# Performance work log

Measured on AMD Instinct MI355X. Metric: run time of the kernel, lower is better.

Reference implementation:

```python
import jax, jax.numpy as jnp
import numpy as np

D = 1024   # visual_dim
N = 64     # num_phrases(1) * topN(64)
DEG = 16   # edges per subject row (incl. one guaranteed via a permutation)
E = N * DEG
T = 2      # cfg.MODEL.RELATION.VISUAL_GRAPH_PASSING_TIME


def _graph():
    rng = np.random.default_rng(0)
    perm = rng.permutation(N)
    mask = np.zeros((N, N), bool)
    for i in range(N):
        mask[i, perm[i]] = True  # permutation guarantees every column is covered
        pool = np.delete(np.arange(N), perm[i])
        mask[i, rng.choice(pool, DEG - 1, replace=False)] = True
    hdim, wdim = np.nonzero(mask)  # row-major, exactly E entries
    conn = np.full((N, N), -1, np.int32)
    conn[hdim, wdim] = np.arange(hdim.shape[0])
    edge_idx = hdim * N + wdim  # original: hdim*topN + wdim (topN == N since num_phrases == 1)
    return conn, edge_idx.astype(np.int32)


def setup_inputs():
    conn, edge_idx = _graph()
    key = jax.random.key(0)
    ks = jax.random.split(key, 16)
    p = lambda k, shp: jax.random.normal(k, shp, jnp.float32) * 0.02
    return {
        'visual_feat': jax.random.normal(ks[0], (N, D), jnp.float32),
        'rel_visual_feat': jax.random.normal(ks[1], (E, D), jnp.float32),
        'conn_map': jnp.asarray(conn),
        'topN_boxes_ids': jnp.arange(N, dtype=jnp.int32)[None, :],  # only shape is used
        'edge_idx': jnp.asarray(edge_idx),
        'W_sub': p(ks[2], (D, D)),
        'W_obj': p(ks[3], (D, D)),
        'W_r2s': p(ks[4], (D, D)),
        'W_r2o': p(ks[5], (D, D)),
        'W_joint': p(ks[6], (D, 4 * D)),
        'W_ctx': p(ks[7], (D, 3 * D)),
        'W_rel_update': p(ks[8], (D, 3 * D)),
        'W_rel_joint': p(ks[9], (D, 4 * D)),
        'W_rel_ctx': p(ks[10], (D, 2 * D)),
        'W_node': p(ks[11], (D, 2 * D)),
        'b_node': jnp.zeros((D,), jnp.float32),
        'W_factor': p(ks[12], (D, 2 * D)),
    }


def _forward(visual_feat, rel_visual_feat, conn_map, edge_idx,
             W_sub, W_obj, W_r2s, W_r2o, W_joint, W_ctx, W_rel_update,
             W_rel_joint, W_rel_ctx, W_node, b_node, W_factor):
    n, d = visual_feat.shape
    scale = jnp.asarray(d, visual_feat.dtype) ** 0.5
    connected = conn_map >= 0
    # scatter edge features into the dense [N, N, D] grid
    rel_temp = (jnp.zeros((n * n, d), visual_feat.dtype)
                .at[edge_idx].set(rel_visual_feat)
                .reshape(n, n, d))
    rel_ctx = rel_temp
    vctx = visual_feat
    for _ in range(T):
        # joint node embedding  [N, D]
        vj = jnp.concatenate([visual_feat, vctx, visual_feat * vctx, vctx - visual_feat], 1) @ W_joint.T
        # joint edge embedding  [N, N, D] (1x1 conv == per-position linear)
        rj = jnp.einsum('ijd,od->ijo',
                        jnp.concatenate([rel_temp, rel_ctx, rel_temp * rel_ctx, rel_temp - rel_ctx], 2),
                        W_rel_joint)
        # node -> edge: cat(sub_tile, obj_tile, rj) @ W_rel_update, done without tiling
        Ws, Wo, Wr = W_rel_update[:, :d], W_rel_update[:, d:2 * d], W_rel_update[:, 2 * d:]
        rel_j = (vj @ Ws.T)[:, None, :] + (vj @ Wo.T)[None, :, :] + jnp.einsum('ijd,od->ijo', rj, Wr)
        # edge -> node attention scores (elementwise product of 1x1-conv outputs, summed over channels)
        s_sbj = jnp.einsum('id,ijd->ij', vj @ W_sub.T, jnp.einsum('ijd,od->ijo', rel_j, W_r2s)) / scale
        s_obj = jnp.einsum('jd,ijd->ij', vj @ W_obj.T, jnp.einsum('ijd,od->ijo', rel_j, W_r2o)) / scale
        w_sbj = jax.nn.softmax(jnp.where(connected, s_sbj, -jnp.inf), axis=1)
        w_obj = jax.nn.softmax(jnp.where(connected, s_obj, -jnp.inf), axis=0)
        ctx = jnp.concatenate([jnp.einsum('ijd,ij->id', rel_j, w_sbj),
                               jnp.einsum('ijd,ij->jd', rel_j, w_obj)], 1)
        vctx = jnp.concatenate([vctx, ctx], 1) @ W_ctx.T
        rel_ctx = jnp.einsum('ijd,od->ijo', jnp.concatenate([rel_ctx, rel_j], 2), W_rel_ctx)
    # gather back the valid edges and produce outputs
    rel_out = jnp.concatenate([rel_visual_feat, rel_ctx.reshape(-1, d)[edge_idx]], 1) @ W_factor.T
    v_out = jnp.concatenate([visual_feat, vctx], 1) @ W_node.T + b_node
    deg = connected.sum(1) + connected.sum(0)
    v_out = jnp.where((deg == 0)[:, None], visual_feat, v_out)  # isolated nodes pass through
    return rel_out, v_out


def reference(visual_feat, rel_visual_feat, conn_map, topN_boxes_ids, edge_idx,
              W_sub, W_obj, W_r2s, W_r2o, W_joint, W_ctx, W_rel_update,
              W_rel_joint, W_rel_ctx, W_node, b_node, W_factor):
    del topN_boxes_ids  # only its shape is used in the original
    return _forward(visual_feat, rel_visual_feat, conn_map, edge_idx,
                    W_sub, W_obj, W_r2s, W_r2o, W_joint, W_ctx, W_rel_update,
                    W_rel_joint, W_rel_ctx, W_node, b_node, W_factor)
```

## Files before the change

### kernel.cpp

```cpp
#include <hip/hip_runtime.h>

static constexpr int kN = 64;
static constexpr int kD = 1024;
static constexpr int kE = 1024;
static constexpr int kT = 2;

typedef short  bf16x8 __attribute__((ext_vector_type(8)));
typedef float  f32x4  __attribute__((ext_vector_type(4)));
typedef unsigned short us8 __attribute__((ext_vector_type(8)));
typedef unsigned short us4 __attribute__((ext_vector_type(4)));

__device__ __forceinline__ unsigned short f2b(float f) {
    unsigned int u = __builtin_bit_cast(unsigned int, f);
    u += 0x7FFFu + ((u >> 16) & 1u);
    return (unsigned short)(u >> 16);
}
__device__ __forceinline__ float b2f(unsigned short u) {
    unsigned int x = ((unsigned int)u) << 16;
    return __builtin_bit_cast(float, x);
}
__device__ __forceinline__ bf16x8 cvt8(float4 a, float4 b) {
    us8 o;
    o[0] = f2b(a.x); o[1] = f2b(a.y); o[2] = f2b(a.z); o[3] = f2b(a.w);
    o[4] = f2b(b.x); o[5] = f2b(b.y); o[6] = f2b(b.z); o[7] = f2b(b.w);
    return __builtin_bit_cast(bf16x8, o);
}

struct ASrc { const unsigned short* s0; const unsigned short* s1; const unsigned short* s2; int mode; };

__device__ __forceinline__ bf16x8 loadA8(const ASrc& s, int row, int kg) {
    const int seg = kg >> 10, k = kg & 1023;
    const size_t ro = (size_t)row * 1024 + k;
    if (s.mode == 1) {
        const unsigned short* p = (seg == 0) ? s.s0 : (seg == 1 ? s.s1 : s.s2);
        return *(const bf16x8*)(p + ro);
    }
    const bf16x8 a = *(const bf16x8*)(s.s0 + ro);
    if (seg == 0) return a;
    const bf16x8 b = *(const bf16x8*)(s.s1 + ro);
    const us8 ua = __builtin_bit_cast(us8, a), ub = __builtin_bit_cast(us8, b);
    us8 o;
#pragma unroll
    for (int q = 0; q < 8; ++q) o[q] = f2b(b2f(ua[q]) * b2f(ub[q]));
    return __builtin_bit_cast(bf16x8, o);
}

struct GJob { ASrc a; const unsigned short* W; int ldw; void* P; int M; int K; int KS; int pbf; };
struct GJobs { GJob j[5]; int t0[6]; int nj; };

__global__ __launch_bounds__(256)
void k_gemm(GJobs G)
{
    __shared__ unsigned short lds[16896];
    const int flat = blockIdx.x;
    int ji = 0;
    while (ji + 1 < G.nj && flat >= G.t0[ji + 1]) ++ji;
    const GJob J = G.j[ji];
    const int local = flat - G.t0[ji];
    const int tid = threadIdx.x, lane = tid & 63, wid = tid >> 6;
    const int l15 = lane & 15, l4 = lane >> 4;
    const int sr = tid >> 3, sc8 = tid & 7;
    const int wc8 = (sc8 ^ (sr & 7)) * 8;

    if (J.M >= 128) {
        const int rowTiles = J.M >> 7;
        const int rt = local % rowTiles;
        const int rest = local / rowTiles;
        const int ct = rest & 7, z = rest >> 3;
        const int rowBase = rt * 128, colBase = ct * 128;
        const int kchunk = J.K / J.KS, kbeg = z * kchunk, kend = kbeg + kchunk;
        const int wr = wid >> 1, wc = wid & 1;

        f32x4 acc[4][4] = {};
        bf16x8 ra[4], rb[4];
        auto stage = [&](int kt) {
#pragma unroll
            for (int h = 0; h < 4; ++h) {
                ra[h] = loadA8(J.a, rowBase + sr + 32 * h, kt + sc8 * 8);
                rb[h] = *(const bf16x8*)(J.W + (size_t)(colBase + sr + 32 * h) * J.ldw + kt + sc8 * 8);
            }
        };

        stage(kbeg);
        for (int kt = kbeg; kt < kend; kt += 64) {
            __syncthreads();
#pragma unroll
            for (int h = 0; h < 4; ++h) {
                *(bf16x8*)&lds[(sr + 32 * h) * 64 + wc8] = ra[h];
                *(bf16x8*)&lds[8192 + (sr + 32 * h) * 64 + wc8] = rb[h];
            }
            __syncthreads();
            if (kt + 64 < kend) stage(kt + 64);
#pragma unroll
            for (int kk = 0; kk < 2; ++kk) {
                bf16x8 af[4], bv[4];
#pragma unroll
                for (int m = 0; m < 4; ++m) {
                    const int ar = wr * 64 + m * 16 + l15;
                    af[m] = *(const bf16x8*)&lds[ar * 64 + (((kk << 2) | l4) ^ (ar & 7)) * 8];
                }
#pragma unroll
                for (int n = 0; n < 4; ++n) {
                    const int br = wc * 64 + n * 16 + l15;
                    bv[n] = *(const bf16x8*)&lds[8192 + br * 64 + (((kk << 2) | l4) ^ (br & 7)) * 8];
                }
#pragma unroll
                for (int m = 0; m < 4; ++m)
#pragma unroll
                    for (int n = 0; n < 4; ++n)
                        acc[m][n] = __builtin_amdgcn_mfma_f32_16x16x32_bf16(af[m], bv[n], acc[m][n], 0, 0, 0);
            }
        }

        __syncthreads();
#pragma unroll
        for (int m = 0; m < 4; ++m)
#pragma unroll
            for (int n = 0; n < 4; ++n)
#pragma unroll
                for (int r = 0; r < 4; ++r)
                    lds[(wr * 64 + m * 16 + l4 * 4 + r) * 132 + wc * 64 + n * 16 + l15] =
                        f2b(acc[m][n][r]);
        __syncthreads();
        unsigned short* Pb = (unsigned short*)J.P + (size_t)z * J.M * 1024;
#pragma unroll
        for (int c = tid; c < 2048; c += 256) {
            const int row = c >> 4, ch = c & 15;
            *(bf16x8*)(Pb + (size_t)(rowBase + row) * 1024 + colBase + ch * 8) =
                *(const bf16x8*)&lds[row * 132 + ch * 8];
        }
    } else {
        const int ct = local & 7, z = local >> 3;
        const int colBase = ct * 128;
        const int kchunk = J.K / J.KS, kbeg = z * kchunk, kend = kbeg + kchunk;
        const int wr = wid >> 1, wc = wid & 1;

        bf16x8 ra[2], rb[4];
        auto stage = [&](int kt) {
#pragma unroll
            for (int h = 0; h < 2; ++h)
                ra[h] = loadA8(J.a, sr + 32 * h, kt + sc8 * 8);
#pragma unroll
            for (int h = 0; h < 4; ++h)
                rb[h] = *(const bf16x8*)(J.W + (size_t)(colBase + sr + 32 * h) * J.ldw + kt + sc8 * 8);
        };

        f32x4 acc[2][4] = {};
        stage(kbeg);
        for (int kt = kbeg; kt < kend; kt += 64) {
            __syncthreads();
#pragma unroll
            for (int h = 0; h < 2; ++h)
                *(bf16x8*)&lds[(sr + 32 * h) * 64 + wc8] = ra[h];
#pragma unroll
            for (int h = 0; h < 4; ++h)
                *(bf16x8*)&lds[4096 + (sr + 32 * h) * 64 + wc8] = rb[h];
            __syncthreads();
            if (kt + 64 < kend) stage(kt + 64);
#pragma unroll
            for (int kk = 0; kk < 2; ++kk) {
                const int c8 = kk * 4 + l4;
                bf16x8 af[2], bv[4];
#pragma unroll
                for (int m = 0; m < 2; ++m) {
                    const int ar = wr * 32 + m * 16 + l15;
                    af[m] = *(const bf16x8*)&lds[ar * 64 + (c8 ^ (ar & 7)) * 8];
                }
#pragma unroll
                for (int n = 0; n < 4; ++n) {
                    const int br = wc * 64 + n * 16 + l15;
                    bv[n] = *(const bf16x8*)&lds[4096 + br * 64 + (c8 ^ (br & 7)) * 8];
                }
#pragma unroll
                for (int m = 0; m < 2; ++m)
#pragma unroll
                    for (int n = 0; n < 4; ++n)
                        acc[m][n] = __builtin_amdgcn_mfma_f32_16x16x32_bf16(af[m], bv[n], acc[m][n], 0, 0, 0);
            }
        }
        float* base = (float*)J.P + (size_t)z * J.M * 1024;
#pragma unroll
        for (int m = 0; m < 2; ++m) {
            const int row = wr * 32 + m * 16 + l4 * 4;
#pragma unroll
            for (int n = 0; n < 4; ++n) {
                const int col = colBase + wc * 64 + n * 16 + l15;
#pragma unroll
                for (int r = 0; r < 4; ++r)
                    base[(size_t)(row + r) * 1024 + col] = acc[m][n][r];
            }
        }
    }
}

struct RJob { const void* P; int MO8; int KS; int pbf; float* Cf; unsigned short* Cb;
              const unsigned short* addb; const float* bias; int gather; };
struct RJobs { RJob j[6]; int t0[7]; int nj; const int* eidx; const float* gP; int gKS; };

__global__ void k_reduce(RJobs R)
{
    const int flat = blockIdx.x;
    int ji = 0;
    while (ji + 1 < R.nj && flat >= R.t0[ji + 1]) ++ji;
    const RJob J = R.j[ji];
    const int i8 = (flat - R.t0[ji]) * 256 + threadIdx.x;
    if (i8 >= J.MO8) return;
    float s[8] = {0.f, 0.f, 0.f, 0.f, 0.f, 0.f, 0.f, 0.f};
    if (J.pbf) {
        const unsigned short* P = (const unsigned short*)J.P;
        for (int z = 0; z < J.KS; ++z) {
            const us8 v = *(const us8*)(P + (size_t)z * J.MO8 * 8 + (size_t)i8 * 8);
#pragma unroll
            for (int q = 0; q < 8; ++q) s[q] += b2f(v[q]);
        }
    } else {
        const float* P = (const float*)J.P;
        for (int z = 0; z < J.KS; ++z) {
            const float* p = P + (size_t)z * J.MO8 * 8 + (size_t)i8 * 8;
            const float4 v0 = *(const float4*)p;
            const float4 v1 = *(const float4*)(p + 4);
            s[0] += v0.x; s[1] += v0.y; s[2] += v0.z; s[3] += v0.w;
            s[4] += v1.x; s[5] += v1.y; s[6] += v1.z; s[7] += v1.w;
        }
    }
    if (J.addb) {
        const us8 v = *(const us8*)(J.addb + (size_t)i8 * 8);
#pragma unroll
        for (int q = 0; q < 8; ++q) s[q] += b2f(v[q]);
    }
    if (J.gather) {
        const int e = i8 >> 7, c8 = i8 & 127;
        const int idx = R.eidx[e];
        const float* as_ = R.gP + (size_t)(idx >> 6) * 1024 + c8 * 8;
        const float* ao_ = R.gP + 131072 + (size_t)(idx & 63) * 1024 + c8 * 8;
        for (int z = 0; z < R.gKS; ++z) {
#pragma unroll
            for (int q = 0; q < 8; ++q)
                s[q] += as_[(size_t)z * 65536 + q] + ao_[(size_t)z * 65536 + q];
        }
    }
    if (J.bias) {
        const int c8 = i8 & 127;
#pragma unroll
        for (int q = 0; q < 8; ++q) s[q] += J.bias[c8 * 8 + q];
    }
    if (J.Cf) {
        *(float4*)(J.Cf + (size_t)i8 * 8)     = make_float4(s[0], s[1], s[2], s[3]);
        *(float4*)(J.Cf + (size_t)i8 * 8 + 4) = make_float4(s[4], s[5], s[6], s[7]);
    }
    if (J.Cb) {
        us8 o;
#pragma unroll
        for (int q = 0; q < 8; ++q) o[q] = f2b(s[q]);
        *(us8*)(J.Cb + (size_t)i8 * 8) = o;
    }
}

struct ConvBatch { const float* s[7]; unsigned short* d[7]; int beg8[7]; int total8; };
__global__ void k_f2b_batch(ConvBatch cb)
{
    int i = blockIdx.x * blockDim.x + threadIdx.x;
    if (i >= cb.total8) return;
    int k = 0;
    while (k < 6 && i >= cb.beg8[k + 1]) ++k;
    const int j = i - cb.beg8[k];
    const float4 v0 = reinterpret_cast<const float4*>(cb.s[k])[2 * j];
    const float4 v1 = reinterpret_cast<const float4*>(cb.s[k])[2 * j + 1];
    const bf16x8 o = cvt8(v0, v1);
    *(bf16x8*)(cb.d[k] + (size_t)j * 8) = o;
}

struct T4 { const float* s[4]; unsigned short* d[4]; };
__global__ __launch_bounds__(256)
void k_transpose(T4 t4)
{
    __shared__ float tile[64][65];
    const float* __restrict__ src = t4.s[blockIdx.z];
    unsigned short* __restrict__ dst = t4.d[blockIdx.z];
    const int bx = blockIdx.x * 64, by = blockIdx.y * 64;
    const int c = threadIdx.x & 63, r0 = threadIdx.x >> 6;
#pragma unroll
    for (int h = 0; h < 16; ++h) {
        const int r = r0 * 16 + h;
        tile[r][c] = src[(size_t)(by + r) * 1024 + bx + c];
    }
    __syncthreads();
#pragma unroll
    for (int h = 0; h < 16; ++h) {
        const int kk = r0 * 16 + h;
        dst[(size_t)(bx + kk) * 1024 + by + c] = f2b(tile[c][kk]);
    }
}

__global__ __launch_bounds__(256)
void k_buildW(const float* __restrict__ Wrel, const float* __restrict__ Wjnt,
              unsigned short* __restrict__ WrtRel, unsigned short* __restrict__ WeffRel,
              unsigned short* __restrict__ UrtVj, unsigned short* __restrict__ UeffVj)
{
    const int idx = blockIdx.x * 256 + threadIdx.x;
    const int o = idx >> 8, j = (idx & 255) * 4;
    const float* W = blockIdx.z ? Wjnt : Wrel;
    const float sgn = blockIdx.z ? -1.f : 1.f;
    unsigned short* rt = blockIdx.z ? UrtVj : WrtRel;
    unsigned short* ef = blockIdx.z ? UeffVj : WeffRel;
    const float4 w1 = *(const float4*)(W + (size_t)o * 4096 + j);
    const float4 w2 = *(const float4*)(W + (size_t)o * 4096 + 1024 + j);
    const float4 w3 = *(const float4*)(W + (size_t)o * 4096 + 2048 + j);
    const float4 w4 = *(const float4*)(W + (size_t)o * 4096 + 3072 + j);
    us4 t;
    t.x = f2b(w1.x + sgn * w4.x); t.y = f2b(w1.y + sgn * w4.y);
    t.z = f2b(w1.z + sgn * w4.z); t.w = f2b(w1.w + sgn * w4.w);
    *(us4*)(rt + (size_t)o * 1024 + j) = t;
    t.x = f2b(w2.x - sgn * w4.x); t.y = f2b(w2.y - sgn * w4.y);
    t.z = f2b(w2.z - sgn * w4.z); t.w = f2b(w2.w - sgn * w4.w);
    *(us4*)(ef + (size_t)o * 2048 + j) = t;
    t.x = f2b(w3.x); t.y = f2b(w3.y); t.z = f2b(w3.z); t.w = f2b(w3.w);
    *(us4*)(ef + (size_t)o * 2048 + 1024 + j) = t;
}

__global__ __launch_bounds__(256)
void k_sctx(const float* __restrict__ relj, const float* __restrict__ qws,
            const float* __restrict__ qwo, const int* __restrict__ conn,
            unsigned short* __restrict__ ctx1b, unsigned short* __restrict__ ctx2b)
{
    const int bid = blockIdx.x, t = threadIdx.x;
    const float4* relj4 = reinterpret_cast<const float4*>(relj);
    __shared__ float sl[64];
    __shared__ int el[64];
    float4 acc = make_float4(0.f, 0.f, 0.f, 0.f);

    if (bid < 64) {
        const int i = bid;
        {
            const int g = t >> 4, l = t & 15;
            const size_t e4 = (size_t)(i * 16 + g) * 256;
            const float4* q4 = reinterpret_cast<const float4*>(qws) + (size_t)i * 256;
            float v = 0.f;
#pragma unroll
            for (int q = 0; q < 16; ++q) {
                const float4 r = relj4[e4 + l + q * 16];
                const float4 a = q4[l + q * 16];
                v += a.x * r.x + a.y * r.y + a.z * r.z + a.w * r.w;
            }
            v += __shfl_xor(v, 1, 16);
            v += __shfl_xor(v, 2, 16);
            v += __shfl_xor(v, 4, 16);
            v += __shfl_xor(v, 8, 16);
            if (l == 0) sl[g] = v * 0.03125f;
        }
        __syncthreads();
        float sv[16];
        float m = -1e30f;
#pragma unroll
        for (int q = 0; q < 16; ++q) { sv[q] = sl[q]; m = fmaxf(m, sv[q]); }
        float sum = 0.f;
#pragma unroll
        for (int q = 0; q < 16; ++q) { sv[q] = expf(sv[q] - m); sum += sv[q]; }
        const float inv = 1.f / sum;
#pragma unroll
        for (int q = 0; q < 16; ++q) {
            const float w = sv[q] * inv;
            const float4 v = relj4[(size_t)(i * 16 + q) * 256 + t];
            acc.x += w * v.x; acc.y += w * v.y; acc.z += w * v.z; acc.w += w * v.w;
        }
        us4 o; o.x = f2b(acc.x); o.y = f2b(acc.y); o.z = f2b(acc.z); o.w = f2b(acc.w);
        *(us4*)(ctx1b + (size_t)i * 1024 + t * 4) = o;
    } else {
        const int j = bid - 64;
        {
            const int i = t >> 2, sub = t & 3;
            const int e = conn[i * kN + j];
            if (sub == 0) el[i] = e;
            float v = 0.f;
            if (e >= 0) {
                const size_t e4 = (size_t)e * 256;
                const float4* q4 = reinterpret_cast<const float4*>(qwo) + (size_t)j * 256;
#pragma unroll
                for (int q = 0; q < 64; ++q) {
                    const float4 r = relj4[e4 + sub + q * 4];
                    const float4 a = q4[sub + q * 4];
                    v += a.x * r.x + a.y * r.y + a.z * r.z + a.w * r.w;
                }
            }
            v += __shfl_xor(v, 1, 4);
            v += __shfl_xor(v, 2, 4);
            if (sub == 0) sl[i] = (e >= 0) ? v * 0.03125f : -1e30f;
        }
        __syncthreads();
        float m = -1e30f;
        for (int i = 0; i < 64; ++i) m = fmaxf(m, sl[i]);
        float sum = 0.f;
        float ex[64];
        for (int i = 0; i < 64; ++i) {
            ex[i] = (el[i] >= 0) ? expf(sl[i] - m) : 0.f;
            sum += ex[i];
        }
        const float inv = 1.f / sum;
        for (int i = 0; i < 64; ++i) {
            const int e = el[i];
            if (e >= 0) {
                const float w = ex[i] * inv;
                const float4 v = relj4[(size_t)e * 256 + t];
                acc.x += w * v.x; acc.y += w * v.y; acc.z += w * v.z; acc.w += w * v.w;
            }
        }
        us4 o; o.x = f2b(acc.x); o.y = f2b(acc.y); o.z = f2b(acc.z); o.w = f2b(acc.w);
        *(us4*)(ctx2b + (size_t)j * 1024 + t * 4) = o;
    }
}

extern "C" void kernel_launch(void* const* d_in, const int* in_sizes, int n_in,
                              void* d_out, int out_size, void* d_ws, size_t ws_size,
                              hipStream_t stream)
{
    const float* visual   = (const float*)d_in[0];
    const float* relvis   = (const float*)d_in[1];
    const int*   conn     = (const int*)d_in[2];
    const int*   edge_idx = (const int*)d_in[4];
    const float* W_sub    = (const float*)d_in[5];
    const float* W_obj    = (const float*)d_in[6];
    const float* W_r2s    = (const float*)d_in[7];
    const float* W_r2o    = (const float*)d_in[8];
    const float* W_joint  = (const float*)d_in[9];
    const float* W_ctx    = (const float*)d_in[10];
    const float* W_relu   = (const float*)d_in[11];
    const float* W_relj   = (const float*)d_in[12];
    const float* W_relc   = (const float*)d_in[13];
    const float* W_node   = (const float*)d_in[14];
    const float* b_node   = (const float*)d_in[15];
    const float* W_factor = (const float*)d_in[16];
    (void)in_sizes; (void)n_in; (void)out_size; (void)ws_size;

    float* ws = (float*)d_ws;
    size_t off = 0;
    auto allocF = [&](size_t n) { float* p = ws + off; off += n; return p; };
    auto allocU = [&](size_t n) { return (unsigned short*)allocF((n + 1) / 2); };

    float* partF = allocF((size_t)1024 * 1024);
    unsigned short* partB = allocU((size_t)16 * 1024 * 1024);
    float* asqw  = allocF((size_t)4 * 64 * 1024);
    float* relj  = allocF((size_t)kE * kD);
    unsigned short* relvis_b = allocU((size_t)kE * kD);
    unsigned short* visual_b = allocU((size_t)kN * kD);
    unsigned short* vj_b   = allocU((size_t)kN * kD);
    unsigned short* rj_b   = allocU((size_t)kE * kD);
    unsigned short* relj_b = allocU((size_t)kE * kD);
    unsigned short* rc_bA  = allocU((size_t)kE * kD);
    unsigned short* rc_bB  = allocU((size_t)kE * kD);
    unsigned short* vctx_bA = allocU((size_t)kN * kD);
    unsigned short* vctx_bB = allocU((size_t)kN * kD);
    unsigned short* ctx1_b = allocU((size_t)kN * kD);
    unsigned short* ctx2_b = allocU((size_t)kN * kD);
    unsigned short* R0_b = allocU((size_t)kE * kD);
    unsigned short* G0_b = allocU((size_t)kN * kD);
    unsigned short* Wb_ctx    = allocU((size_t)kD * 3 * kD);
    unsigned short* Wb_relu   = allocU((size_t)kD * 3 * kD);
    unsigned short* Wb_relc   = allocU((size_t)kD * 2 * kD);
    unsigned short* Wb_node   = allocU((size_t)kD * 2 * kD);
    unsigned short* Wb_factor = allocU((size_t)kD * 2 * kD);
    unsigned short* WsubT = allocU((size_t)kD * kD);
    unsigned short* WobjT = allocU((size_t)kD * kD);
    unsigned short* Wr2sT = allocU((size_t)kD * kD);
    unsigned short* Wr2oT = allocU((size_t)kD * kD);
    unsigned short* Wc_s  = allocU((size_t)kD * kD);
    unsigned short* Wc_o  = allocU((size_t)kD * kD);
    unsigned short* WrtRel  = allocU((size_t)kD * kD);
    unsigned short* WeffRel = allocU((size_t)kD * 2 * kD);
    unsigned short* UrtVj   = allocU((size_t)kD * kD);
    unsigned short* UeffVj  = allocU((size_t)kD * 2 * kD);

    auto seg1 = [](const unsigned short* a) {
        ASrc s; s.s0 = a; s.s1 = nullptr; s.s2 = nullptr; s.mode = 1; return s;
    };
    auto seg2 = [](const unsigned short* a, const unsigned short* b) {
        ASrc s; s.s0 = a; s.s1 = b; s.s2 = nullptr; s.mode = 1; return s;
    };
    auto seg3 = [](const unsigned short* a, const unsigned short* b, const unsigned short* c) {
        ASrc s; s.s0 = a; s.s1 = b; s.s2 = c; s.mode = 1; return s;
    };
    auto prodA = [](const unsigned short* c, const unsigned short* x) {
        ASrc s; s.s0 = c; s.s1 = x; s.s2 = nullptr; s.mode = 2; return s;
    };

    GJobs G; RJobs R;
    int gn = 0, gt = 0, rn = 0, rtt = 0;
    auto gAdd = [&](ASrc a, const unsigned short* W, int ldw, void* P, int M, int K, int KS, int pbf) {
        G.j[gn].a = a; G.j[gn].W = W; G.j[gn].ldw = ldw; G.j[gn].P = P;
        G.j[gn].M = M; G.j[gn].K = K; G.j[gn].KS = KS; G.j[gn].pbf = pbf;
        G.t0[gn] = gt;
        gt += (M >= 128) ? KS * (M >> 7) * 8 : KS * 8;
        ++gn;
    };
    auto gLaunch = [&]() {
        G.nj = gn; G.t0[gn] = gt;
        hipLaunchKernelGGL(k_gemm, dim3(gt), dim3(256), 0, stream, G);
        gn = 0; gt = 0;
    };
    auto rAdd = [&](const void* P, int MO8, int KS, int pbf, float* Cf, unsigned short* Cb,
                    const unsigned short* addb, const float* bias, int gather) {
        R.j[rn].P = P; R.j[rn].MO8 = MO8; R.j[rn].KS = KS; R.j[rn].pbf = pbf;
        R.j[rn].Cf = Cf; R.j[rn].Cb = Cb; R.j[rn].addb = addb; R.j[rn].bias = bias;
        R.j[rn].gather = gather;
        R.t0[rn] = rtt; rtt += (MO8 + 255) / 256; ++rn;
    };
    auto rLaunch = [&](const int* eidx, const float* gP, int gKS) {
        R.nj = rn; R.t0[rn] = rtt; R.eidx = eidx; R.gP = gP; R.gKS = gKS;
        hipLaunchKernelGGL(k_reduce, dim3(rtt), dim3(256), 0, stream, R);
        rn = 0; rtt = 0;
    };

    {
        ConvBatch cb;
        const float* srcs[7] = {W_ctx, W_relu, W_relc, W_node, W_factor, relvis, visual};
        unsigned short* dsts[7] = {Wb_ctx, Wb_relu, Wb_relc, Wb_node, Wb_factor, relvis_b, visual_b};
        const int nel[7] = {3 * 1024 * 1024, 3 * 1024 * 1024, 2 * 1024 * 1024,
                            2 * 1024 * 1024, 2 * 1024 * 1024, 1024 * 1024, 64 * 1024};
        int cum = 0;
        for (int k = 0; k < 7; ++k) { cb.s[k] = srcs[k]; cb.d[k] = dsts[k]; cb.beg8[k] = cum; cum += nel[k] / 8; }
        cb.total8 = cum;
        hipLaunchKernelGGL(k_f2b_batch, dim3((cum + 255) / 256), dim3(256), 0, stream, cb);
    }
    {
        T4 t4;
        t4.s[0] = W_sub; t4.d[0] = WsubT;
        t4.s[1] = W_obj; t4.d[1] = WobjT;
        t4.s[2] = W_r2s; t4.d[2] = Wr2sT;
        t4.s[3] = W_r2o; t4.d[3] = Wr2oT;
        hipLaunchKernelGGL(k_transpose, dim3(16, 16, 4), dim3(256), 0, stream, t4);
    }
    hipLaunchKernelGGL(k_buildW, dim3(1024, 1, 2), dim3(256), 0, stream,
                       W_relj, W_joint, WrtRel, WeffRel, UrtVj, UeffVj);

    const size_t PB1 = (size_t)4 * 1024 * 1024;
    gAdd(seg1(Wr2sT), WsubT, 1024, partB, 1024, 1024, 4, 1);
    gAdd(seg1(Wr2oT), WobjT, 1024, partB + PB1, 1024, 1024, 4, 1);
    gAdd(seg1(relvis_b), WrtRel, 1024, partB + 2 * PB1, 1024, 1024, 4, 1);
    gAdd(seg1(visual_b), UrtVj, 1024, partF, 64, 1024, 4, 0);
    gLaunch();
    rAdd(partB, 131072, 4, 1, nullptr, Wc_s, nullptr, nullptr, 0);
    rAdd(partB + PB1, 131072, 4, 1, nullptr, Wc_o, nullptr, nullptr, 0);
    rAdd(partB + 2 * PB1, 131072, 4, 1, nullptr, R0_b, nullptr, nullptr, 0);
    rAdd(partF, 8192, 4, 0, nullptr, G0_b, nullptr, nullptr, 0);
    rLaunch(nullptr, nullptr, 0);

    for (int t = 0; t < kT; ++t) {
        const unsigned short* vcur  = (t == 0) ? visual_b : vctx_bA;
        unsigned short*       vnext = (t == 0) ? vctx_bA : vctx_bB;
        const unsigned short* rccur = (t == 0) ? relvis_b : rc_bA;
        unsigned short*       rcnext = (t == 0) ? rc_bA : rc_bB;

        gAdd(prodA(vcur, visual_b), UeffVj, 2048, partF, 64, 2048, 8, 0);
        gAdd(prodA(rccur, relvis_b), WeffRel, 2048, partB, 1024, 2048, 8, 1);
        gLaunch();
        rAdd(partF, 8192, 8, 0, nullptr, vj_b, G0_b, nullptr, 0);
        rAdd(partB, 131072, 8, 1, nullptr, rj_b, R0_b, nullptr, 0);
        rLaunch(nullptr, nullptr, 0);

        gAdd(seg1(vj_b), Wb_relu,        3072, partF,          64, 1024, 2, 0);
        gAdd(seg1(vj_b), Wb_relu + 1024, 3072, partF + 131072, 64, 1024, 2, 0);
        gAdd(seg1(vj_b), Wc_s,           1024, partF + 262144, 64, 1024, 2, 0);
        gAdd(seg1(vj_b), Wc_o,           1024, partF + 393216, 64, 1024, 2, 0);
        gAdd(seg1(rj_b), Wb_relu + 2048, 3072, partB,        1024, 1024, 4, 1);
        gLaunch();
        rAdd(partF,          8192, 2, 0, asqw,          nullptr, nullptr, nullptr, 0);
        rAdd(partF + 131072, 8192, 2, 0, asqw + 65536,  nullptr, nullptr, nullptr, 0);
        rAdd(partF + 262144, 8192, 2, 0, asqw + 131072, nullptr, nullptr, nullptr, 0);
        rAdd(partF + 393216, 8192, 2, 0, asqw + 196608, nullptr, nullptr, nullptr, 0);
        rAdd(partB, 131072, 4, 1, relj, relj_b, nullptr, nullptr, 1);
        rLaunch(edge_idx, partF, 2);

        hipLaunchKernelGGL(k_sctx, dim3(128), dim3(256), 0, stream,
                           relj, asqw + 131072, asqw + 196608, conn, ctx1_b, ctx2_b);

        gAdd(seg3(vcur, ctx1_b, ctx2_b), Wb_ctx, 3072, partF, 64, 3072, 8, 0);
        gAdd(seg2(rccur, relj_b), Wb_relc, 2048, partB, 1024, 2048, 8, 1);
        gLaunch();
        rAdd(partF, 8192, 8, 0, nullptr, vnext, nullptr, nullptr, 0);
        rAdd(partB, 131072, 8, 1, nullptr, rcnext, nullptr, nullptr, 0);
        rLaunch(nullptr, nullptr, 0);
    }

    float* rel_out = (float*)d_out;
    float* v_out   = (float*)d_out + (size_t)kE * kD;
    gAdd(seg2(relvis_b, rc_bB), Wb_factor, 2048, partB, 1024, 2048, 4, 1);
    gAdd(seg2(visual_b, vctx_bB), Wb_node, 2048, partF, 64, 2048, 8, 0);
    gLaunch();
    rAdd(partB, 131072, 4, 1, rel_out, nullptr, nullptr, nullptr, 0);
    rAdd(partF, 8192, 8, 0, v_out, nullptr, nullptr, b_node, 0);
    rLaunch(nullptr, nullptr, 0);
}
```

Measured before the change: 230.0 us.

## Fold relation-context weight into precomputed products to shorten the critical chain

The second half of the relation-context weight is pre-multiplied with the relation-update weight slices once per call. That turns the rel_ctx update into a GEMM on rj plus gathered per-node terms, launched alongside the relation-update GEMM instead of after the context step. This removes one dependent GEMM/reduce stage per iteration and the relj_b bf16 intermediate. The GEMM kernel is also unified onto a single 64-row tile path, with split-K changed for the setup GEMMs. In exchange it adds extra weight-prep GEMMs and transposes per call and changes bf16 rounding order.

```diff
diff --git a/kernel.cpp b/kernel.cpp
--- a/kernel.cpp
+++ b/kernel.cpp
@@ -26,11 +26,12 @@
     return __builtin_bit_cast(bf16x8, o);
 }
 
-struct ASrc { const unsigned short* s0; const unsigned short* s1; const unsigned short* s2; int mode; };
+struct ASrc { const unsigned short* s0; const unsigned short* s1; const unsigned short* s2;
+              int mode; int ld; };
 
 __device__ __forceinline__ bf16x8 loadA8(const ASrc& s, int row, int kg) {
     const int seg = kg >> 10, k = kg & 1023;
-    const size_t ro = (size_t)row * 1024 + k;
+    const size_t ro = (size_t)row * s.ld + k;
     if (s.mode == 1) {
         const unsigned short* p = (seg == 0) ? s.s0 : (seg == 1 ? s.s1 : s.s2);
         return *(const bf16x8*)(p + ro);
@@ -46,142 +47,97 @@
 }
 
 struct GJob { ASrc a; const unsigned short* W; int ldw; void* P; int M; int K; int KS; int pbf; };
-struct GJobs { GJob j[5]; int t0[6]; int nj; };
+struct GJobs { GJob j[8]; int t0[9]; int nj; };
 
 __global__ __launch_bounds__(256)
 void k_gemm(GJobs G)
 {
-    __shared__ unsigned short lds[16896];
+    __shared__ unsigned short lds[12288];
     const int flat = blockIdx.x;
     int ji = 0;
     while (ji + 1 < G.nj && flat >= G.t0[ji + 1]) ++ji;
     const GJob J = G.j[ji];
     const int local = flat - G.t0[ji];
+    const int rowTiles = J.M >> 6;
+    const int rt = local & (rowTiles - 1);
+    const int rest = local / rowTiles;
+    const int ct = rest & 7, z = rest >> 3;
+    const int rowBase = rt * 64, colBase = ct * 128;
+    const int kchunk = J.K / J.KS, kbeg = z * kchunk, kend = kbeg + kchunk;
+
     const int tid = threadIdx.x, lane = tid & 63, wid = tid >> 6;
     const int l15 = lane & 15, l4 = lane >> 4;
     const int sr = tid >> 3, sc8 = tid & 7;
     const int wc8 = (sc8 ^ (sr & 7)) * 8;
-
-    if (J.M >= 128) {
-        const int rowTiles = J.M >> 7;
-        const int rt = local % rowTiles;
-        const int rest = local / rowTiles;
-        const int ct = rest & 7, z = rest >> 3;
-        const int rowBase = rt * 128, colBase = ct * 128;
-        const int kchunk = J.K / J.KS, kbeg = z * kchunk, kend = kbeg + kchunk;
-        const int wr = wid >> 1, wc = wid & 1;
-
-        f32x4 acc[4][4] = {};
-        bf16x8 ra[4], rb[4];
-        auto stage = [&](int kt) {
-#pragma unroll
-            for (int h = 0; h < 4; ++h) {
-                ra[h] = loadA8(J.a, rowBase + sr + 32 * h, kt + sc8 * 8);
-                rb[h] = *(const bf16x8*)(J.W + (size_t)(colBase + sr + 32 * h) * J.ldw + kt + sc8 * 8);
+    const int wr = wid >> 1, wc = wid & 1;
+
+    bf16x8 ra[2], rb[4];
+    auto stage = [&](int kt) {
+#pragma unroll
+        for (int h = 0; h < 2; ++h)
+            ra[h] = loadA8(J.a, rowBase + sr + 32 * h, kt + sc8 * 8);
+#pragma unroll
+        for (int h = 0; h < 4; ++h)
+            rb[h] = *(const bf16x8*)(J.W + (size_t)(colBase + sr + 32 * h) * J.ldw + kt + sc8 * 8);
+    };
+
+    f32x4 acc[2][4] = {};
+    stage(kbeg);
+    for (int kt = kbeg; kt < kend; kt += 64) {
+        __syncthreads();
+#pragma unroll
+        for (int h = 0; h < 2; ++h)
+            *(bf16x8*)&lds[(sr + 32 * h) * 64 + wc8] = ra[h];
+#pragma unroll
+        for (int h = 0; h < 4; ++h)
+            *(bf16x8*)&lds[4096 + (sr + 32 * h) * 64 + wc8] = rb[h];
+        __syncthreads();
+        if (kt + 64 < kend) stage(kt + 64);
+#pragma unroll
+        for (int kk = 0; kk < 2; ++kk) {
+            const int c8 = kk * 4 + l4;
+            bf16x8 af[2], bv[4];
+#pragma unroll
+            for (int m = 0; m < 2; ++m) {
+                const int ar = wr * 32 + m * 16 + l15;
+                af[m] = *(const bf16x8*)&lds[ar * 64 + (c8 ^ (ar & 7)) * 8];
             }
-        };
-
-        stage(kbeg);
-        for (int kt = kbeg; kt < kend; kt += 64) {
-            __syncthreads();
-#pragma unroll
-            for (int h = 0; h < 4; ++h) {
-                *(bf16x8*)&lds[(sr + 32 * h) * 64 + wc8] = ra[h];
-                *(bf16x8*)&lds[8192 + (sr + 32 * h) * 64 + wc8] = rb[h];
+#pragma unroll
+            for (int n = 0; n < 4; ++n) {
+                const int br = wc * 64 + n * 16 + l15;
+                bv[n] = *(const bf16x8*)&lds[4096 + br * 64 + (c8 ^ (br & 7)) * 8];
             }
-            __syncthreads();
-            if (kt + 64 < kend) stage(kt + 64);
-#pragma unroll
-            for (int kk = 0; kk < 2; ++kk) {
-                bf16x8 af[4], bv[4];
-#pragma unroll
-                for (int m = 0; m < 4; ++m) {
-                    const int ar = wr * 64 + m * 16 + l15;
-                    af[m] = *(const bf16x8*)&lds[ar * 64 + (((kk << 2) | l4) ^ (ar & 7)) * 8];
-                }
-#pragma unroll
-                for (int n = 0; n < 4; ++n) {
-                    const int br = wc * 64 + n * 16 + l15;
-                    bv[n] = *(const bf16x8*)&lds[8192 + br * 64 + (((kk << 2) | l4) ^ (br & 7)) * 8];
-                }
-#pragma unroll
-                for (int m = 0; m < 4; ++m)
-#pragma unroll
-                    for (int n = 0; n < 4; ++n)
-                        acc[m][n] = __builtin_amdgcn_mfma_f32_16x16x32_bf16(af[m], bv[n], acc[m][n], 0, 0, 0);
-            }
-        }
-
+#pragma unroll
+            for (int m = 0; m < 2; ++m)
+#pragma unroll
+                for (int n = 0; n < 4; ++n)
+                    acc[m][n] = __builtin_amdgcn_mfma_f32_16x16x32_bf16(af[m], bv[n], acc[m][n], 0, 0, 0);
+        }
+    }
+
+    if (J.pbf) {
         __syncthreads();
 #pragma unroll
-        for (int m = 0; m < 4; ++m)
+        for (int m = 0; m < 2; ++m)
 #pragma unroll
             for (int n = 0; n < 4; ++n)
 #pragma unroll
                 for (int r = 0; r < 4; ++r)
-                    lds[(wr * 64 + m * 16 + l4 * 4 + r) * 132 + wc * 64 + n * 16 + l15] =
+                    lds[(wr * 32 + m * 16 + l4 * 4 + r) * 132 + wc * 64 + n * 16 + l15] =
                         f2b(acc[m][n][r]);
         __syncthreads();
         unsigned short* Pb = (unsigned short*)J.P + (size_t)z * J.M * 1024;
 #pragma unroll
-        for (int c = tid; c < 2048; c += 256) {
+        for (int c = tid; c < 1024; c += 256) {
             const int row = c >> 4, ch = c & 15;
             *(bf16x8*)(Pb + (size_t)(rowBase + row) * 1024 + colBase + ch * 8) =
                 *(const bf16x8*)&lds[row * 132 + ch * 8];
         }
     } else {
-        const int ct = local & 7, z = local >> 3;
-        const int colBase = ct * 128;
-        const int kchunk = J.K / J.KS, kbeg = z * kchunk, kend = kbeg + kchunk;
-        const int wr = wid >> 1, wc = wid & 1;
-
-        bf16x8 ra[2], rb[4];
-        auto stage = [&](int kt) {
-#pragma unroll
-            for (int h = 0; h < 2; ++h)
-                ra[h] = loadA8(J.a, sr + 32 * h, kt + sc8 * 8);
-#pragma unroll
-            for (int h = 0; h < 4; ++h)
-                rb[h] = *(const bf16x8*)(J.W + (size_t)(colBase + sr + 32 * h) * J.ldw + kt + sc8 * 8);
-        };
-
-        f32x4 acc[2][4] = {};
-        stage(kbeg);
-        for (int kt = kbeg; kt < kend; kt += 64) {
-            __syncthreads();
-#pragma unroll
-            for (int h = 0; h < 2; ++h)
-                *(bf16x8*)&lds[(sr + 32 * h) * 64 + wc8] = ra[h];
-#pragma unroll
-            for (int h = 0; h < 4; ++h)
-                *(bf16x8*)&lds[4096 + (sr + 32 * h) * 64 + wc8] = rb[h];
-            __syncthreads();
-            if (kt + 64 < kend) stage(kt + 64);
-#pragma unroll
-            for (int kk = 0; kk < 2; ++kk) {
-                const int c8 = kk * 4 + l4;
-                bf16x8 af[2], bv[4];
-#pragma unroll
-                for (int m = 0; m < 2; ++m) {
-                    const int ar = wr * 32 + m * 16 + l15;
-                    af[m] = *(const bf16x8*)&lds[ar * 64 + (c8 ^ (ar & 7)) * 8];
-                }
-#pragma unroll
-                for (int n = 0; n < 4; ++n) {
-                    const int br = wc * 64 + n * 16 + l15;
-                    bv[n] = *(const bf16x8*)&lds[4096 + br * 64 + (c8 ^ (br & 7)) * 8];
-                }
-#pragma unroll
-                for (int m = 0; m < 2; ++m)
-#pragma unroll
-                    for (int n = 0; n < 4; ++n)
-                        acc[m][n] = __builtin_amdgcn_mfma_f32_16x16x32_bf16(af[m], bv[n], acc[m][n], 0, 0, 0);
-            }
-        }
         float* base = (float*)J.P + (size_t)z * J.M * 1024;
 #pragma unroll
         for (int m = 0; m < 2; ++m) {
-            const int row = wr * 32 + m * 16 + l4 * 4;
+            const int row = rowBase + wr * 32 + m * 16 + l4 * 4;
 #pragma unroll
             for (int n = 0; n < 4; ++n) {
                 const int col = colBase + wc * 64 + n * 16 + l15;
@@ -194,8 +150,9 @@
 }
 
 struct RJob { const void* P; int MO8; int KS; int pbf; float* Cf; unsigned short* Cb;
-              const unsigned short* addb; const float* bias; int gather; };
-struct RJobs { RJob j[6]; int t0[7]; int nj; const int* eidx; const float* gP; int gKS; };
+              const unsigned short* addb; const float* bias; int gather;
+              const float* gP; int ostride; };
+struct RJobs { RJob j[8]; int t0[9]; int nj; const int* eidx; int gKS; };
 
 __global__ void k_reduce(RJobs R)
 {
@@ -231,8 +188,8 @@
     if (J.gather) {
         const int e = i8 >> 7, c8 = i8 & 127;
         const int idx = R.eidx[e];
-        const float* as_ = R.gP + (size_t)(idx >> 6) * 1024 + c8 * 8;
-        const float* ao_ = R.gP + 131072 + (size_t)(idx & 63) * 1024 + c8 * 8;
+        const float* as_ = J.gP + (size_t)(idx >> 6) * 1024 + c8 * 8;
+        const float* ao_ = J.gP + 131072 + (size_t)(idx & 63) * 1024 + c8 * 8;
         for (int z = 0; z < R.gKS; ++z) {
 #pragma unroll
             for (int q = 0; q < 8; ++q)
@@ -252,7 +209,12 @@
         us8 o;
 #pragma unroll
         for (int q = 0; q < 8; ++q) o[q] = f2b(s[q]);
-        *(us8*)(J.Cb + (size_t)i8 * 8) = o;
+        if (J.ostride) {
+            const int row = i8 >> 7, c8 = i8 & 127;
+            *(us8*)(J.Cb + (size_t)row * J.ostride + c8 * 8) = o;
+        } else {
+            *(us8*)(J.Cb + (size_t)i8 * 8) = o;
+        }
     }
 }
 
@@ -270,25 +232,25 @@
     *(bf16x8*)(cb.d[k] + (size_t)j * 8) = o;
 }
 
-struct T4 { const float* s[4]; unsigned short* d[4]; };
+struct TJ { const float* s; unsigned short* d; int ld; };
+struct T7 { TJ t[7]; };
 __global__ __launch_bounds__(256)
-void k_transpose(T4 t4)
+void k_transpose(T7 t7)
 {
     __shared__ float tile[64][65];
-    const float* __restrict__ src = t4.s[blockIdx.z];
-    unsigned short* __restrict__ dst = t4.d[blockIdx.z];
+    const TJ tj = t7.t[blockIdx.z];
     const int bx = blockIdx.x * 64, by = blockIdx.y * 64;
     const int c = threadIdx.x & 63, r0 = threadIdx.x >> 6;
 #pragma unroll
     for (int h = 0; h < 16; ++h) {
         const int r = r0 * 16 + h;
-        tile[r][c] = src[(size_t)(by + r) * 1024 + bx + c];
+        tile[r][c] = tj.s[(size_t)(by + r) * tj.ld + bx + c];
     }
     __syncthreads();
 #pragma unroll
     for (int h = 0; h < 16; ++h) {
         const int kk = r0 * 16 + h;
-        dst[(size_t)(bx + kk) * 1024 + by + c] = f2b(tile[c][kk]);
+        tj.d[(size_t)(bx + kk) * 1024 + by + c] = f2b(tile[c][kk]);
     }
 }
 
@@ -444,7 +406,6 @@
     unsigned short* visual_b = allocU((size_t)kN * kD);
     unsigned short* vj_b   = allocU((size_t)kN * kD);
     unsigned short* rj_b   = allocU((size_t)kE * kD);
-    unsigned short* relj_b = allocU((size_t)kE * kD);
     unsigned short* rc_bA  = allocU((size_t)kE * kD);
     unsigned short* rc_bB  = allocU((size_t)kE * kD);
     unsigned short* vctx_bA = allocU((size_t)kN * kD);
@@ -462,24 +423,29 @@
     unsigned short* WobjT = allocU((size_t)kD * kD);
     unsigned short* Wr2sT = allocU((size_t)kD * kD);
     unsigned short* Wr2oT = allocU((size_t)kD * kD);
+    unsigned short* WsT   = allocU((size_t)kD * kD);
+    unsigned short* WoT   = allocU((size_t)kD * kD);
+    unsigned short* WrT   = allocU((size_t)kD * kD);
     unsigned short* Wc_s  = allocU((size_t)kD * kD);
     unsigned short* Wc_o  = allocU((size_t)kD * kD);
+    unsigned short* Wso2  = allocU((size_t)kD * kD);
+    unsigned short* Woo2  = allocU((size_t)kD * kD);
     unsigned short* WrtRel  = allocU((size_t)kD * kD);
     unsigned short* WeffRel = allocU((size_t)kD * 2 * kD);
     unsigned short* UrtVj   = allocU((size_t)kD * kD);
     unsigned short* UeffVj  = allocU((size_t)kD * 2 * kD);
 
-    auto seg1 = [](const unsigned short* a) {
-        ASrc s; s.s0 = a; s.s1 = nullptr; s.s2 = nullptr; s.mode = 1; return s;
+    auto seg1 = [](const unsigned short* a, int ld = 1024) {
+        ASrc s; s.s0 = a; s.s1 = nullptr; s.s2 = nullptr; s.mode = 1; s.ld = ld; return s;
     };
     auto seg2 = [](const unsigned short* a, const unsigned short* b) {
-        ASrc s; s.s0 = a; s.s1 = b; s.s2 = nullptr; s.mode = 1; return s;
+        ASrc s; s.s0 = a; s.s1 = b; s.s2 = nullptr; s.mode = 1; s.ld = 1024; return s;
     };
     auto seg3 = [](const unsigned short* a, const unsigned short* b, const unsigned short* c) {
-        ASrc s; s.s0 = a; s.s1 = b; s.s2 = c; s.mode = 1; return s;
+        ASrc s; s.s0 = a; s.s1 = b; s.s2 = c; s.mode = 1; s.ld = 1024; return s;
     };
     auto prodA = [](const unsigned short* c, const unsigned short* x) {
-        ASrc s; s.s0 = c; s.s1 = x; s.s2 = nullptr; s.mode = 2; return s;
+        ASrc s; s.s0 = c; s.s1 = x; s.s2 = nullptr; s.mode = 2; s.ld = 1024; return s;
     };
 
     GJobs G; RJobs R;
@@ -487,9 +453,7 @@
     auto gAdd = [&](ASrc a, const unsigned short* W, int ldw, void* P, int M, int K, int KS, int pbf) {
         G.j[gn].a = a; G.j[gn].W = W; G.j[gn].ldw = ldw; G.j[gn].P = P;
         G.j[gn].M = M; G.j[gn].K = K; G.j[gn].KS = KS; G.j[gn].pbf = pbf;
-        G.t0[gn] = gt;
-        gt += (M >= 128) ? KS * (M >> 7) * 8 : KS * 8;
-        ++gn;
+        G.t0[gn] = gt; gt += KS * (M >> 6) * 8; ++gn;
     };
     auto gLaunch = [&]() {
         G.nj = gn; G.t0[gn] = gt;
@@ -497,14 +461,15 @@
         gn = 0; gt = 0;
     };
     auto rAdd = [&](const void* P, int MO8, int KS, int pbf, float* Cf, unsigned short* Cb,
-                    const unsigned short* addb, const float* bias, int gather) {
+                    const unsigned short* addb, const float* bias,
+                    const float* gP, int ostride) {
         R.j[rn].P = P; R.j[rn].MO8 = MO8; R.j[rn].KS = KS; R.j[rn].pbf = pbf;
         R.j[rn].Cf = Cf; R.j[rn].Cb = Cb; R.j[rn].addb = addb; R.j[rn].bias = bias;
-        R.j[rn].gather = gather;
+        R.j[rn].gather = (gP != nullptr); R.j[rn].gP = gP; R.j[rn].ostride = ostride;
         R.t0[rn] = rtt; rtt += (MO8 + 255) / 256; ++rn;
     };
-    auto rLaunch = [&](const int* eidx, const float* gP, int gKS) {
-        R.nj = rn; R.t0[rn] = rtt; R.eidx = eidx; R.gP = gP; R.gKS = gKS;
+    auto rLaunch = [&](const int* eidx, int gKS) {
+        R.nj = rn; R.t0[rn] = rtt; R.eidx = eidx; R.gKS = gKS;
         hipLaunchKernelGGL(k_reduce, dim3(rtt), dim3(256), 0, stream, R);
         rn = 0; rtt = 0;
     };
@@ -521,27 +486,36 @@
         hipLaunchKernelGGL(k_f2b_batch, dim3((cum + 255) / 256), dim3(256), 0, stream, cb);
     }
     {
-        T4 t4;
-        t4.s[0] = W_sub; t4.d[0] = WsubT;
-        t4.s[1] = W_obj; t4.d[1] = WobjT;
-        t4.s[2] = W_r2s; t4.d[2] = Wr2sT;
-        t4.s[3] = W_r2o; t4.d[3] = Wr2oT;
-        hipLaunchKernelGGL(k_transpose, dim3(16, 16, 4), dim3(256), 0, stream, t4);
+        T7 t7;
+        t7.t[0] = {W_sub, WsubT, 1024};
+        t7.t[1] = {W_obj, WobjT, 1024};
+        t7.t[2] = {W_r2s, Wr2sT, 1024};
+        t7.t[3] = {W_r2o, Wr2oT, 1024};
+        t7.t[4] = {W_relu,        WsT, 3072};
+        t7.t[5] = {W_relu + 1024, WoT, 3072};
+        t7.t[6] = {W_relu + 2048, WrT, 3072};
+        hipLaunchKernelGGL(k_transpose, dim3(16, 16, 7), dim3(256), 0, stream, t7);
     }
     hipLaunchKernelGGL(k_buildW, dim3(1024, 1, 2), dim3(256), 0, stream,
                        W_relj, W_joint, WrtRel, WeffRel, UrtVj, UeffVj);
 
-    const size_t PB1 = (size_t)4 * 1024 * 1024;
-    gAdd(seg1(Wr2sT), WsubT, 1024, partB, 1024, 1024, 4, 1);
-    gAdd(seg1(Wr2oT), WobjT, 1024, partB + PB1, 1024, 1024, 4, 1);
-    gAdd(seg1(relvis_b), WrtRel, 1024, partB + 2 * PB1, 1024, 1024, 4, 1);
+    const size_t PB2 = (size_t)2 * 1024 * 1024;
+    gAdd(seg1(Wr2sT), WsubT, 1024, partB,           1024, 1024, 2, 1);
+    gAdd(seg1(Wr2oT), WobjT, 1024, partB + PB2,     1024, 1024, 2, 1);
+    gAdd(seg1(relvis_b), WrtRel, 1024, partB + 2 * PB2, 1024, 1024, 2, 1);
+    gAdd(seg1(Wb_relc + 1024, 2048), WrT, 1024, partB + 3 * PB2, 1024, 1024, 2, 1);
+    gAdd(seg1(Wb_relc + 1024, 2048), WsT, 1024, partB + 4 * PB2, 1024, 1024, 2, 1);
+    gAdd(seg1(Wb_relc + 1024, 2048), WoT, 1024, partB + 5 * PB2, 1024, 1024, 2, 1);
     gAdd(seg1(visual_b), UrtVj, 1024, partF, 64, 1024, 4, 0);
     gLaunch();
-    rAdd(partB, 131072, 4, 1, nullptr, Wc_s, nullptr, nullptr, 0);
-    rAdd(partB + PB1, 131072, 4, 1, nullptr, Wc_o, nullptr, nullptr, 0);
-    rAdd(partB + 2 * PB1, 131072, 4, 1, nullptr, R0_b, nullptr, nullptr, 0);
-    rAdd(partF, 8192, 4, 0, nullptr, G0_b, nullptr, nullptr, 0);
-    rLaunch(nullptr, nullptr, 0);
+    rAdd(partB,           131072, 2, 1, nullptr, Wc_s, nullptr, nullptr, nullptr, 0);
+    rAdd(partB + PB2,     131072, 2, 1, nullptr, Wc_o, nullptr, nullptr, nullptr, 0);
+    rAdd(partB + 2 * PB2, 131072, 2, 1, nullptr, R0_b, nullptr, nullptr, nullptr, 0);
+    rAdd(partB + 3 * PB2, 131072, 2, 1, nullptr, Wb_relc + 1024, nullptr, nullptr, nullptr, 2048);
+    rAdd(partB + 4 * PB2, 131072, 2, 1, nullptr, Wso2, nullptr, nullptr, nullptr, 0);
+    rAdd(partB + 5 * PB2, 131072, 2, 1, nullptr, Woo2, nullptr, nullptr, nullptr, 0);
+    rAdd(partF, 8192, 4, 0, nullptr, G0_b, nullptr, nullptr, nullptr, 0);
+    rLaunch(nullptr, 0);
 
     for (int t = 0; t < kT; ++t) {
         const unsigned short* vcur  = (t == 0) ? visual_b : vctx_bA;
@@ -552,32 +526,32 @@
         gAdd(prodA(vcur, visual_b), UeffVj, 2048, partF, 64, 2048, 8, 0);
         gAdd(prodA(rccur, relvis_b), WeffRel, 2048, partB, 1024, 2048, 8, 1);
         gLaunch();
-        rAdd(partF, 8192, 8, 0, nullptr, vj_b, G0_b, nullptr, 0);
-        rAdd(partB, 131072, 8, 1, nullptr, rj_b, R0_b, nullptr, 0);
-        rLaunch(nullptr, nullptr, 0);
+        rAdd(partF, 8192, 8, 0, nullptr, vj_b, G0_b, nullptr, nullptr, 0);
+        rAdd(partB, 131072, 8, 1, nullptr, rj_b, R0_b, nullptr, nullptr, 0);
+        rLaunch(nullptr, 0);
 
         gAdd(seg1(vj_b), Wb_relu,        3072, partF,          64, 1024, 2, 0);
         gAdd(seg1(vj_b), Wb_relu + 1024, 3072, partF + 131072, 64, 1024, 2, 0);
         gAdd(seg1(vj_b), Wc_s,           1024, partF + 262144, 64, 1024, 2, 0);
         gAdd(seg1(vj_b), Wc_o,           1024, partF + 393216, 64, 1024, 2, 0);
+        gAdd(seg1(vj_b), Wso2,           1024, partF + 524288, 64, 1024, 2, 0);
+        gAdd(seg1(vj_b), Woo2,           1024, partF + 655360, 64, 1024, 2, 0);
         gAdd(seg1(rj_b), Wb_relu + 2048, 3072, partB,        1024, 1024, 4, 1);
+        gAdd(seg2(rccur, rj_b), Wb_relc, 2048, partB + 8388608, 1024, 2048, 8, 1);
         gLaunch();
-        rAdd(partF,          8192, 2, 0, asqw,          nullptr, nullptr, nullptr, 0);
-        rAdd(partF + 131072, 8192, 2, 0, asqw + 65536,  nullptr, nullptr, nullptr, 0);
-        rAdd(partF + 262144, 8192, 2, 0, asqw + 131072, nullptr, nullptr, nullptr, 0);
-        rAdd(partF + 393216, 8192, 2, 0, asqw + 196608, nullptr, nullptr, nullptr, 0);
-        rAdd(partB, 131072, 4, 1, relj, relj_b, nullptr, nullptr, 1);
-        rLaunch(edge_idx, partF, 2);
+        rAdd(partF + 262144, 8192, 2, 0, asqw + 131072, nullptr, nullptr, nullptr, nullptr, 0);
+        rAdd(partF + 393216, 8192, 2, 0, asqw + 196608, nullptr, nullptr, nullptr, nullptr, 0);
+        rAdd(partB, 131072, 4, 1, relj, nullptr, nullptr, nullptr, partF, 0);
+        rAdd(partB + 8388608, 131072, 8, 1, nullptr, rcnext, nullptr, nullptr, partF + 524288, 0);
+        rLaunch(edge_idx, 2);
 
         hipLaunchKernelGGL(k_sctx, dim3(128), dim3(256), 0, stream,
                            relj, asqw + 131072, asqw + 196608, conn, ctx1_b, ctx2_b);
 
         gAdd(seg3(vcur, ctx1_b, ctx2_b), Wb_ctx, 3072, partF, 64, 3072, 8, 0);
-        gAdd(seg2(rccur, relj_b), Wb_relc, 2048, partB, 1024, 2048, 8, 1);
         gLaunch();
-        rAdd(partF, 8192, 8, 0, nullptr, vnext, nullptr, nullptr, 0);
-        rAdd(partB, 131072, 8, 1, nullptr, rcnext, nullptr, nullptr, 0);
-        rLaunch(nullptr, nullptr, 0);
+        rAdd(partF, 8192, 8, 0, nullptr, vnext, nullptr, nullptr, nullptr, 0);
+        rLaunch(nullptr, 0);
     }
 
     float* rel_out = (float*)d_out;
@@ -585,7 +559,7 @@
     gAdd(seg2(relvis_b, rc_bB), Wb_factor, 2048, partB, 1024, 2048, 4, 1);
     gAdd(seg2(visual_b, vctx_bB), Wb_node, 2048, partF, 64, 2048, 8, 0);
     gLaunch();
-    rAdd(partB, 131072, 4, 1, rel_out, nullptr, nullptr, nullptr, 0);
-    rAdd(partF, 8192, 8, 0, v_out, nullptr, nullptr, b_node, 0);
-    rLaunch(nullptr, nullptr, 0);
-}
+    rAdd(partB, 131072, 4, 1, rel_out, nullptr, nullptr, nullptr, nullptr, 0);
+    rAdd(partF, 8192, 8, 0, v_out, nullptr, nullptr, b_node, nullptr, 0);
+    rLaunch(nullptr, 0);
+}
```

Result: no change. 233.3 us (+1.4%).
